# Optimization experiments

Hardware: AMD Instinct MI355X
Metric: run time of the kernel (lower is better)

## Reference

```python
import jax, jax.numpy as jnp
import numpy as np
import math

B, C, IMG, P = 16, 3, 512, 16
H = 384            # hidden_size
NH = 6             # num heads
DH = H // NH       # head dim = 64
L = 12             # layers
I = 1536           # intermediate
NC = 1000          # classes
NP = (IMG // P) ** 2          # 1024 patches
S = NP + 1                    # seq len with cls token
EPS = 1e-5
GELU_C = math.sqrt(2.0 / math.pi)


def setup_inputs() -> dict:
    key = jax.random.key(0)
    ks = iter(jax.random.split(key, 32))
    def rn(shape, scale=0.02):
        return (jax.random.normal(next(ks), shape, dtype=jnp.float32) * scale)
    return {
        "x": jax.random.normal(next(ks), (B, C, IMG, IMG), dtype=jnp.float32),
        "conv_w": rn((H, C, P, P)),
        "conv_b": rn((H,)),
        "cls_token": rn((1, 1, H), 1.0),
        "pos_emb": rn((1, S, H), 1.0),
        "ln1_w": jnp.ones((L, H), jnp.float32),
        "ln1_b": jnp.zeros((L, H), jnp.float32),
        "wq": rn((L, H, H)), "bq": rn((L, H)),
        "wk": rn((L, H, H)), "bk": rn((L, H)),
        "wv": rn((L, H, H)), "bv": rn((L, H)),
        "wo": rn((L, H, H)), "bo": rn((L, H)),
        "ln2_w": jnp.ones((L, H), jnp.float32),
        "ln2_b": jnp.zeros((L, H), jnp.float32),
        "w1": rn((L, H, I)), "b1": rn((L, I)),
        "w2": rn((L, I, H)), "b2": rn((L, H)),
        "wc": rn((H, NC)), "bc": rn((NC,)),
    }


def _layernorm(h, w, b):
    mu = jnp.mean(h, axis=-1, keepdims=True)
    var = jnp.mean(jnp.square(h - mu), axis=-1, keepdims=True)
    return (h - mu) * jax.lax.rsqrt(var + EPS) * w + b


def _new_gelu(u):
    return 0.5 * u * (1.0 + jnp.tanh(GELU_C * (u + 0.044715 * u ** 3)))


def _block(h, p):
    (l1w, l1b, wq, bq, wk, bk, wv, bv, wo, bo, l2w, l2b, w1, b1, w2, b2) = p
    hn = _layernorm(h, l1w, l1b)
    q = (hn @ wq + bq).reshape(B, S, NH, DH)
    k = (hn @ wk + bk).reshape(B, S, NH, DH)
    v = (hn @ wv + bv).reshape(B, S, NH, DH)
    scores = jnp.einsum('bihd,bjhd->bhij', q, k) / math.sqrt(DH)
    probs = jax.nn.softmax(scores, axis=-1)
    attn = jnp.einsum('bhij,bjhd->bihd', probs, v).reshape(B, S, H)
    h = h + attn @ wo + bo
    hn = _layernorm(h, l2w, l2b)
    h = h + _new_gelu(hn @ w1 + b1) @ w2 + b2
    return h, None


def reference(x, conv_w, conv_b, cls_token, pos_emb,
              ln1_w, ln1_b, wq, bq, wk, bk, wv, bv, wo, bo,
              ln2_w, ln2_b, w1, b1, w2, b2, wc, bc):
    # Patch embed: stride==kernel conv as einsum over non-overlapping patches
    nh = IMG // P
    patches = x.reshape(B, C, nh, P, nh, P)
    emb = jnp.einsum('bcipjq,ocpq->bijo', patches, conv_w) + conv_b  # [B,nh,nh,H]
    emb = emb.reshape(B, NP, H)
    cls = jnp.broadcast_to(cls_token, (B, 1, H))
    h = jnp.concatenate([cls, emb], axis=1) + pos_emb  # [B,S,H]

    params = (ln1_w, ln1_b, wq, bq, wk, bk, wv, bv, wo, bo,
              ln2_w, ln2_b, w1, b1, w2, b2)
    h, _ = jax.lax.scan(_block, h, params)
    logits = h[:, 0] @ wc + bc  # [B, NC]
    return logits
```

## Files before the change

### kernel.cpp

```cpp
#include <hip/hip_runtime.h>
#include <hip/hip_bf16.h>
#include <math.h>

#define BB 16
#define HH 384
#define NHEAD 6
#define DH 64
#define LL 12
#define II 1536
#define NC 1000
#define SS 1025
#define MROWS (BB * SS)
#define MPAD  16512
#define KPATCH 768
#define MPATCH (BB * 1024)
#define QS 1152
#define SSP 1088

typedef __hip_bfloat16 bf16;
typedef __attribute__((ext_vector_type(8))) short bh8;
typedef __attribute__((ext_vector_type(4))) float f4x;

__device__ __forceinline__ void gload16(const bf16* g, bf16* l) {
    __builtin_amdgcn_global_load_lds(
        (const __attribute__((address_space(1))) unsigned int*)g,
        (__attribute__((address_space(3))) unsigned int*)l, 16, 0, 0);
}

__device__ __forceinline__ unsigned short bf16_bits(float f) {
    __hip_bfloat16 h = __float2bfloat16(f);
    return *reinterpret_cast<unsigned short*>(&h);
}
__device__ __forceinline__ ushort4 pack4_bf16(float a, float b, float c, float d) {
    ushort4 u;
    u.x = bf16_bits(a); u.y = bf16_bits(b); u.z = bf16_bits(c); u.w = bf16_bits(d);
    return u;
}

__global__ __launch_bounds__(256) void transpose_cast_kernel(
    const float* __restrict__ in, bf16* __restrict__ out, int K, int N, int ostride)
{
    __shared__ float tile[32][33];
    int l = blockIdx.z;
    const float* ip = in + (size_t)l * K * N;
    bf16* op = out + (size_t)l * ostride;
    int n0 = blockIdx.x * 32, k0 = blockIdx.y * 32;
    int tx = threadIdx.x & 31, ty = threadIdx.x >> 5;
    #pragma unroll
    for (int i = 0; i < 32; i += 8)
        tile[ty + i][tx] = ip[(size_t)(k0 + ty + i) * N + n0 + tx];
    __syncthreads();
    #pragma unroll
    for (int i = 0; i < 32; i += 8)
        op[(size_t)(n0 + ty + i) * K + k0 + tx] = __float2bfloat16(tile[tx][ty + i]);
}

__global__ __launch_bounds__(256) void cast_kernel(
    const float* __restrict__ in, bf16* __restrict__ out, int n)
{
    int i = blockIdx.x * 1024 + threadIdx.x * 4;
    if (i + 3 < n) {
        float4 v = *(const float4*)&in[i];
        out[i]   = __float2bfloat16(v.x);
        out[i+1] = __float2bfloat16(v.y);
        out[i+2] = __float2bfloat16(v.z);
        out[i+3] = __float2bfloat16(v.w);
    } else {
        for (int j = i; j < n; ++j) out[j] = __float2bfloat16(in[j]);
    }
}

__global__ __launch_bounds__(384) void bias_concat_kernel(
    const float* __restrict__ bq, const float* __restrict__ bk,
    const float* __restrict__ bv, float* __restrict__ cb)
{
    int l = blockIdx.x, t = threadIdx.x;
    cb[l * QS + t]       = bq[l * HH + t];
    cb[l * QS + 384 + t] = bk[l * HH + t];
    cb[l * QS + 768 + t] = bv[l * HH + t];
}

__global__ __launch_bounds__(256) void im2row_kernel(
    const float* __restrict__ x, bf16* __restrict__ Pm)
{
    size_t idx = ((size_t)blockIdx.x * 256 + threadIdx.x) * 8;
    int kk = (int)(idx % KPATCH);
    int m  = (int)(idx / KPATCH);
    int b = m >> 10, p = m & 1023;
    int c = kk >> 8, rem = kk & 255, py = rem >> 4, px = rem & 15;
    int pi = p >> 5, pj = p & 31;
    const float* src = &x[(((size_t)b * 3 + c) * 512 + pi * 16 + py) * 512 + pj * 16 + px];
    float4 a0 = *(const float4*)src;
    float4 a1 = *(const float4*)(src + 4);
    bf16 tmp[8];
    tmp[0] = __float2bfloat16(a0.x); tmp[1] = __float2bfloat16(a0.y);
    tmp[2] = __float2bfloat16(a0.z); tmp[3] = __float2bfloat16(a0.w);
    tmp[4] = __float2bfloat16(a1.x); tmp[5] = __float2bfloat16(a1.y);
    tmp[6] = __float2bfloat16(a1.z); tmp[7] = __float2bfloat16(a1.w);
    *(bh8*)&Pm[idx] = *(bh8*)tmp;
}

__global__ __launch_bounds__(384) void fill_cls_kernel(
    const float* __restrict__ cls, const float* __restrict__ pos, float* __restrict__ h)
{
    h[(size_t)blockIdx.x * SS * HH + threadIdx.x] = cls[threadIdx.x] + pos[threadIdx.x];
}

__global__ __launch_bounds__(256) void ln_kernel(
    const float* __restrict__ x, const float* __restrict__ w,
    const float* __restrict__ b, bf16* __restrict__ out, int nrows)
{
    int wave = threadIdx.x >> 6;
    int lane = threadIdx.x & 63;
    int row = blockIdx.x * 4 + wave;
    if (row >= nrows) return;
    const float* xr = x + (size_t)row * HH;
    float vals[6];
    float s = 0.f;
    #pragma unroll
    for (int i = 0; i < 6; ++i) { vals[i] = xr[lane + 64 * i]; s += vals[i]; }
    #pragma unroll
    for (int mask = 32; mask >= 1; mask >>= 1) s += __shfl_xor(s, mask);
    float mean = s * (1.f / HH);
    float vs = 0.f;
    #pragma unroll
    for (int i = 0; i < 6; ++i) { float d = vals[i] - mean; vs += d * d; }
    #pragma unroll
    for (int mask = 32; mask >= 1; mask >>= 1) vs += __shfl_xor(vs, mask);
    float rstd = rsqrtf(vs * (1.f / HH) + 1e-5f);
    bf16* outr = out + (size_t)row * HH;
    #pragma unroll
    for (int i = 0; i < 6; ++i) {
        int jj = lane + 64 * i;
        outr[jj] = __float2bfloat16((vals[i] - mean) * rstd * w[jj] + b[jj]);
    }
}

__global__ __launch_bounds__(256) void vt_kernel(
    const bf16* __restrict__ qkv, bf16* __restrict__ vt)
{
    __shared__ bf16 tile[32][33];
    int bh = blockIdx.z;
    int b = bh / NHEAD, hd = bh % NHEAD;
    int s0 = blockIdx.x * 32, d0 = blockIdx.y * 32;
    int tx = threadIdx.x & 31, ty = threadIdx.x >> 5;
    const bf16* src = qkv + ((size_t)b * SS) * QS + 768 + hd * DH;
    #pragma unroll
    for (int i = 0; i < 32; i += 8) {
        int s = s0 + ty + i;
        tile[ty + i][tx] = (s < SS) ? src[(size_t)s * QS + d0 + tx]
                                    : __float2bfloat16(0.f);
    }
    __syncthreads();
    #pragma unroll
    for (int i = 0; i < 32; i += 8)
        vt[((size_t)bh * DH + d0 + ty + i) * SSP + s0 + tx] = tile[tx][ty + i];
}

template<int MODE>
__global__ __launch_bounds__(256) void gemm_v2_kernel(
    const bf16* __restrict__ A, const bf16* __restrict__ Bt,
    const float* __restrict__ bias, const float* __restrict__ res,
    void* __restrict__ out, int M, int N, int K)
{
    __shared__ bf16 As[128 * 64];
    __shared__ bf16 Bs[128 * 64];

    int t = threadIdx.x;
    int w = t >> 6, lane = t & 63;
    int quad = lane >> 4, l15 = lane & 15;
    int bm = blockIdx.x * 128, bn = blockIdx.y * 128;
    int wm = (w >> 1) * 64, wn = (w & 1) * 64;

    int srow = lane >> 3;
    int scol = lane & 7;

    f4x acc[4][4];
    #pragma unroll
    for (int i = 0; i < 4; ++i)
        #pragma unroll
        for (int j = 0; j < 4; ++j) acc[i][j] = 0.f;

    for (int k0 = 0; k0 < K; k0 += 64) {
        #pragma unroll
        for (int p = 0; p < 4; ++p) {
            int c = w * 4 + p;
            int r = c * 8 + srow;
            int gcb = scol ^ (r & 7);
            gload16(A + (size_t)(bm + r) * K + k0 + gcb * 8, &As[c * 8 * 64]);
        }
        #pragma unroll
        for (int p = 0; p < 4; ++p) {
            int c = w * 4 + p;
            int r = c * 8 + srow;
            int gcb = scol ^ (r & 7);
            gload16(Bt + (size_t)(bn + r) * K + k0 + gcb * 8, &Bs[c * 8 * 64]);
        }
        __syncthreads();

        #pragma unroll
        for (int kc = 0; kc < 2; ++kc) {
            bh8 bfr[4];
            #pragma unroll
            for (int nf = 0; nf < 4; ++nf) {
                int rn = wn + nf * 16 + l15;
                int pcb = (kc * 4 + quad) ^ (rn & 7);
                bfr[nf] = *(const bh8*)&Bs[rn * 64 + pcb * 8];
            }
            #pragma unroll
            for (int mf = 0; mf < 4; ++mf) {
                int rm = wm + mf * 16 + l15;
                int pcb = (kc * 4 + quad) ^ (rm & 7);
                bh8 afr = *(const bh8*)&As[rm * 64 + pcb * 8];
                #pragma unroll
                for (int nf = 0; nf < 4; ++nf)
                    acc[mf][nf] = __builtin_amdgcn_mfma_f32_16x16x32_bf16(
                        bfr[nf], afr, acc[mf][nf], 0, 0, 0);
            }
        }
        __syncthreads();
    }

    #pragma unroll
    for (int mf = 0; mf < 4; ++mf) {
        int row = bm + wm + mf * 16 + l15;
        #pragma unroll
        for (int nf = 0; nf < 4; ++nf) {
            f4x v = acc[mf][nf];
            int col0 = bn + wn + nf * 16 + quad * 4;
            float4 b4 = *(const float4*)&bias[col0];
            float vals[4];
            #pragma unroll
            for (int r = 0; r < 4; ++r) vals[r] = v[r] + (&b4.x)[r];
            if (MODE == 0) {
                if (row < M)
                    *(ushort4*)&((bf16*)out)[(size_t)row * N + col0] =
                        pack4_bf16(vals[0], vals[1], vals[2], vals[3]);
            } else if (MODE == 1) {
                #pragma unroll
                for (int r = 0; r < 4; ++r) {
                    float u = vals[r];
                    float z = 0.7978845608028654f * (u + 0.044715f * u * u * u);
                    z = fminf(fmaxf(z, -15.f), 15.f);
                    float e = __expf(2.f * z);
                    vals[r] = 0.5f * u * (1.f + (e - 1.f) / (e + 1.f));
                }
                if (row < M)
                    *(ushort4*)&((bf16*)out)[(size_t)row * N + col0] =
                        pack4_bf16(vals[0], vals[1], vals[2], vals[3]);
            } else if (MODE == 2) {
                if (row < M) {
                    float* o = (float*)out;
                    float4 r4 = *(const float4*)&res[(size_t)row * N + col0];
                    float4 st = {vals[0] + r4.x, vals[1] + r4.y,
                                 vals[2] + r4.z, vals[3] + r4.w};
                    *(float4*)&o[(size_t)row * N + col0] = st;
                }
            } else {
                int b2 = row >> 10, p2 = row & 1023;
                size_t orow = (size_t)b2 * SS + 1 + p2;
                float4 r4 = *(const float4*)&res[(size_t)(1 + p2) * HH + col0];
                float4 st = {vals[0] + r4.x, vals[1] + r4.y,
                             vals[2] + r4.z, vals[3] + r4.w};
                *(float4*)&((float*)out)[orow * HH + col0] = st;
            }
        }
    }
}

#define PSTR 68

__global__ __launch_bounds__(256) void attn_v4_kernel(
    const bf16* __restrict__ qkv, const bf16* __restrict__ vt,
    bf16* __restrict__ o)
{
    __shared__ bf16 Qs[64 * 64];
    __shared__ bf16 Ks[64 * 64];
    __shared__ bf16 Vs[64 * 64];
    __shared__ bf16 Ps[4][16 * PSTR];

    int t = threadIdx.x, w = t >> 6, lane = t & 63;
    int quad = lane >> 4, l15 = lane & 15;
    int bh = blockIdx.x;
    int b = bh / NHEAD, hd = bh % NHEAD;
    int q0 = blockIdx.y * 64;
    size_t qbase = ((size_t)b * SS) * QS + hd * DH;
    size_t kbase = qbase + 384;
    size_t vbase = (size_t)bh * DH * SSP;
    size_t obase = ((size_t)b * SS) * HH + hd * DH;

    int srow = lane >> 3, scol = lane & 7;
    int gcb = scol ^ srow;

    #pragma unroll
    for (int p = 0; p < 2; ++p) {
        int c = w * 2 + p;
        int r = c * 8 + srow;
        gload16(qkv + qbase + (size_t)(q0 + r) * QS + gcb * 8, &Qs[c * 512]);
    }
    __syncthreads();

    bh8 qfrag[2];
    {
        int rm = 16 * w + l15;
        #pragma unroll
        for (int kc = 0; kc < 2; ++kc)
            qfrag[kc] = *(const bh8*)&Qs[rm * 64 + ((kc * 4 + quad) ^ (rm & 7)) * 8];
    }

    f4x oacc[4];
    #pragma unroll
    for (int i = 0; i < 4; ++i) oacc[i] = 0.f;
    float l_part = 0.f;

    const float C1 = 0.18033688011112042f;
    const float C2 = -16.0f;

    for (int c0 = 0; c0 < SS; c0 += 64) {
        __syncthreads();
        #pragma unroll
        for (int p = 0; p < 2; ++p) {
            int c = w * 2 + p;
            int r = c * 8 + srow;
            gload16(qkv + kbase + (size_t)(c0 + r) * QS + gcb * 8, &Ks[c * 512]);
            gload16(vt + vbase + (size_t)r * SSP + c0 + gcb * 8, &Vs[c * 512]);
        }
        __syncthreads();

        bool tail = (c0 + 64 > SS);
        #pragma unroll
        for (int nf = 0; nf < 4; ++nf) {
            f4x s = 0.f;
            int rn = nf * 16 + l15;
            #pragma unroll
            for (int kc = 0; kc < 2; ++kc) {
                bh8 kf = *(const bh8*)&Ks[rn * 64 + ((kc * 4 + quad) ^ (rn & 7)) * 8];
                s = __builtin_amdgcn_mfma_f32_16x16x32_bf16(kf, qfrag[kc], s, 0, 0, 0);
            }
            float pv[4];
            #pragma unroll
            for (int r = 0; r < 4; ++r) {
                float p = exp2f(fmaf(s[r], C1, C2));
                if (tail && (c0 + nf * 16 + quad * 4 + r >= SS)) p = 0.f;
                pv[r] = p;
                l_part += p;
            }
            *(ushort4*)&Ps[w][l15 * PSTR + nf * 16 + quad * 4] =
                pack4_bf16(pv[0], pv[1], pv[2], pv[3]);
        }

        bh8 pf[2];
        #pragma unroll
        for (int kc = 0; kc < 2; ++kc)
            pf[kc] = *(const bh8*)&Ps[w][l15 * PSTR + kc * 32 + quad * 8];

        #pragma unroll
        for (int nf2 = 0; nf2 < 4; ++nf2) {
            int rn2 = nf2 * 16 + l15;
            #pragma unroll
            for (int kc = 0; kc < 2; ++kc) {
                bh8 vf = *(const bh8*)&Vs[rn2 * 64 + ((kc * 4 + quad) ^ (rn2 & 7)) * 8];
                oacc[nf2] = __builtin_amdgcn_mfma_f32_16x16x32_bf16(vf, pf[kc], oacc[nf2], 0, 0, 0);
            }
        }
    }

    l_part += __shfl_xor(l_part, 16);
    l_part += __shfl_xor(l_part, 32);
    float inv = 1.f / l_part;

    int row = q0 + 16 * w + l15;
    if (row < SS) {
        #pragma unroll
        for (int nf2 = 0; nf2 < 4; ++nf2) {
            *(ushort4*)&o[obase + (size_t)row * HH + nf2 * 16 + quad * 4] =
                pack4_bf16(oacc[nf2][0] * inv, oacc[nf2][1] * inv,
                           oacc[nf2][2] * inv, oacc[nf2][3] * inv);
        }
    }
}

__global__ __launch_bounds__(256) void cls_kernel(
    const float* __restrict__ h, const float* __restrict__ wc,
    const float* __restrict__ bc, float* __restrict__ out)
{
    __shared__ float hr[HH];
    __shared__ float part[4][64];
    int b = blockIdx.y, n0 = blockIdx.x * 64;
    int t = threadIdx.x;
    for (int i = t; i < HH; i += 256) hr[i] = h[(size_t)b * SS * HH + i];
    __syncthreads();
    int nn = t & 63, seg = t >> 6;
    int n = n0 + nn;
    float acc = 0.f;
    if (n < NC) {
        #pragma unroll 4
        for (int kk = seg * 96; kk < seg * 96 + 96; ++kk)
            acc += hr[kk] * wc[(size_t)kk * NC + n];
    }
    part[seg][nn] = acc;
    __syncthreads();
    if (t < 64 && n0 + t < NC)
        out[b * NC + n0 + t] = part[0][t] + part[1][t] + part[2][t] + part[3][t] + bc[n0 + t];
}

extern "C" void kernel_launch(void* const* d_in, const int* in_sizes, int n_in,
                              void* d_out, int out_size, void* d_ws, size_t ws_size,
                              hipStream_t stream) {
    const float* x        = (const float*)d_in[0];
    const float* conv_w   = (const float*)d_in[1];
    const float* conv_b   = (const float*)d_in[2];
    const float* cls_tok  = (const float*)d_in[3];
    const float* pos_emb  = (const float*)d_in[4];
    const float* ln1_w    = (const float*)d_in[5];
    const float* ln1_b    = (const float*)d_in[6];
    const float* wq       = (const float*)d_in[7];
    const float* bq       = (const float*)d_in[8];
    const float* wk       = (const float*)d_in[9];
    const float* bk       = (const float*)d_in[10];
    const float* wv       = (const float*)d_in[11];
    const float* bv       = (const float*)d_in[12];
    const float* wo       = (const float*)d_in[13];
    const float* bo       = (const float*)d_in[14];
    const float* ln2_w    = (const float*)d_in[15];
    const float* ln2_b    = (const float*)d_in[16];
    const float* w1       = (const float*)d_in[17];
    const float* b1       = (const float*)d_in[18];
    const float* w2       = (const float*)d_in[19];
    const float* b2       = (const float*)d_in[20];
    const float* wc       = (const float*)d_in[21];
    const float* bc       = (const float*)d_in[22];
    float* out = (float*)d_out;

    char* wp = (char*)d_ws;
    float* h   = (float*)wp;  wp += (size_t)MROWS * HH * 4;
    bf16* hn   = (bf16*)wp;
    bf16* vtb  = (bf16*)wp;   wp += (size_t)96 * DH * SSP * 2;
    bf16* tb   = (bf16*)wp;   wp += (size_t)MPAD * HH * 2;
    bf16* mb   = (bf16*)wp;   wp += (size_t)MPAD * II * 2;
    bf16* qkvb = mb;
    bf16* Pm   = mb;
    bf16* wqkv = (bf16*)wp;   wp += (size_t)LL * QS * HH * 2;
    bf16* wot  = (bf16*)wp;   wp += (size_t)LL * HH * HH * 2;
    bf16* w1t  = (bf16*)wp;   wp += (size_t)LL * HH * II * 2;
    bf16* w2t  = (bf16*)wp;   wp += (size_t)LL * II * HH * 2;
    bf16* cwb  = (bf16*)wp;   wp += (size_t)HH * KPATCH * 2;
    float* cbias = (float*)wp; wp += (size_t)LL * QS * 4;

    transpose_cast_kernel<<<dim3(12, 12, LL), 256, 0, stream>>>(wq, wqkv,          HH, HH, QS * HH);
    transpose_cast_kernel<<<dim3(12, 12, LL), 256, 0, stream>>>(wk, wqkv + 147456, HH, HH, QS * HH);
    transpose_cast_kernel<<<dim3(12, 12, LL), 256, 0, stream>>>(wv, wqkv + 294912, HH, HH, QS * HH);
    transpose_cast_kernel<<<dim3(12, 12, LL), 256, 0, stream>>>(wo, wot, HH, HH, HH * HH);
    transpose_cast_kernel<<<dim3(48, 12, LL), 256, 0, stream>>>(w1, w1t, HH, II, HH * II);
    transpose_cast_kernel<<<dim3(12, 48, LL), 256, 0, stream>>>(w2, w2t, II, HH, II * HH);
    cast_kernel<<<288, 256, 0, stream>>>(conv_w, cwb, HH * KPATCH);
    bias_concat_kernel<<<LL, 384, 0, stream>>>(bq, bk, bv, cbias);

    im2row_kernel<<<6144, 256, 0, stream>>>(x, Pm);
    gemm_v2_kernel<3><<<dim3(128, 3), 256, 0, stream>>>(
        Pm, cwb, conv_b, pos_emb, h, MPATCH, HH, KPATCH);
    fill_cls_kernel<<<BB, 384, 0, stream>>>(cls_tok, pos_emb, h);

    const int M = MROWS;
    dim3 gQKV(129, 9);
    dim3 gH(129, 3);
    dim3 gI(129, 12);

    for (int l = 0; l < LL; ++l) {
        const float* l1w = ln1_w + (size_t)l * HH;
        const float* l1b = ln1_b + (size_t)l * HH;
        const float* l2w = ln2_w + (size_t)l * HH;
        const float* l2b = ln2_b + (size_t)l * HH;
        const bf16* wqkv_l = wqkv + (size_t)l * QS * HH;
        const bf16* wo_l   = wot  + (size_t)l * HH * HH;
        const bf16* w1_l   = w1t  + (size_t)l * HH * II;
        const bf16* w2_l   = w2t  + (size_t)l * II * HH;
        const float* cb_l  = cbias + (size_t)l * QS;
        const float* bo_l  = bo + (size_t)l * HH;
        const float* b1_l  = b1 + (size_t)l * II;
        const float* b2_l  = b2 + (size_t)l * HH;

        ln_kernel<<<4100, 256, 0, stream>>>(h, l1w, l1b, hn, M);

        gemm_v2_kernel<0><<<gQKV, 256, 0, stream>>>(hn, wqkv_l, cb_l, nullptr, qkvb, M, QS, HH);

        vt_kernel<<<dim3(33, 2, 96), 256, 0, stream>>>(qkvb, vtb);

        attn_v4_kernel<<<dim3(96, 17), 256, 0, stream>>>(qkvb, vtb, tb);

        gemm_v2_kernel<2><<<gH, 256, 0, stream>>>(tb, wo_l, bo_l, h, h, M, HH, HH);

        ln_kernel<<<4100, 256, 0, stream>>>(h, l2w, l2b, hn, M);

        gemm_v2_kernel<1><<<gI, 256, 0, stream>>>(hn, w1_l, b1_l, nullptr, mb, M, II, HH);
        gemm_v2_kernel<2><<<gH, 256, 0, stream>>>(mb, w2_l, b2_l, h, h, M, HH, II);
    }

    cls_kernel<<<dim3(16, BB), 256, 0, stream>>>(h, wc, bc, out);
}
```

Before: 3.264 ms.

## Process 128 query rows per attention block and compute softmax sum via MFMA

The attention kernel now handles two 64-row query bands per block, so each K/V tile loaded into LDS is reused twice and the grid drops from 17 to 9 query blocks. The row sum of probabilities is computed by an extra MFMA against a ones row appended to the V tile, replacing per-lane accumulation and shuffles. The Q and P buffers share one LDS region, and the tail mask is hoisted out of the common path. The trade-offs are fewer blocks per head, which lowers parallelism, and higher register pressure from doubled accumulators. The sum is also now taken from bf16-rounded probabilities.

Result: slower. 3.398 ms (+4.1%).

```diff
diff --git a/kernel.cpp b/kernel.cpp
--- a/kernel.cpp
+++ b/kernel.cpp
@@ -270,20 +270,19 @@
 
 #define PSTR 68
 
-__global__ __launch_bounds__(256) void attn_v4_kernel(
+__global__ __launch_bounds__(256) void attn_v5_kernel(
     const bf16* __restrict__ qkv, const bf16* __restrict__ vt,
     bf16* __restrict__ o)
 {
-    __shared__ bf16 Qs[64 * 64];
+    __shared__ bf16 QPs[8704];
     __shared__ bf16 Ks[64 * 64];
-    __shared__ bf16 Vs[64 * 64];
-    __shared__ bf16 Ps[4][16 * PSTR];
+    __shared__ bf16 Vs[80 * 64];
 
     int t = threadIdx.x, w = t >> 6, lane = t & 63;
     int quad = lane >> 4, l15 = lane & 15;
     int bh = blockIdx.x;
     int b = bh / NHEAD, hd = bh % NHEAD;
-    int q0 = blockIdx.y * 64;
+    int q0 = blockIdx.y * 128;
     size_t qbase = ((size_t)b * SS) * QS + hd * DH;
     size_t kbase = qbase + 384;
     size_t vbase = (size_t)bh * DH * SSP;
@@ -293,25 +292,32 @@
     int gcb = scol ^ srow;
 
     #pragma unroll
-    for (int p = 0; p < 2; ++p) {
-        int c = w * 2 + p;
+    for (int p = 0; p < 4; ++p) {
+        int c = w * 4 + p;
         int r = c * 8 + srow;
-        gload16(qkv + qbase + (size_t)(q0 + r) * QS + gcb * 8, &Qs[c * 512]);
-    }
+        gload16(qkv + qbase + (size_t)(q0 + r) * QS + gcb * 8, &QPs[c * 512]);
+    }
+    for (int i = t; i < 16 * 64; i += 256)
+        Vs[64 * 64 + i] = __float2bfloat16(i < 64 ? 1.f : 0.f);
     __syncthreads();
 
-    bh8 qfrag[2];
-    {
-        int rm = 16 * w + l15;
+    bh8 qfrag[2][2];
+    #pragma unroll
+    for (int band = 0; band < 2; ++band) {
+        int rm = band * 64 + 16 * w + l15;
         #pragma unroll
         for (int kc = 0; kc < 2; ++kc)
-            qfrag[kc] = *(const bh8*)&Qs[rm * 64 + ((kc * 4 + quad) ^ (rm & 7)) * 8];
-    }
-
-    f4x oacc[4];
-    #pragma unroll
-    for (int i = 0; i < 4; ++i) oacc[i] = 0.f;
-    float l_part = 0.f;
+            qfrag[band][kc] = *(const bh8*)&QPs[rm * 64 + ((kc * 4 + quad) ^ (rm & 7)) * 8];
+    }
+
+    f4x oacc[2][4];
+    f4x oacc_l[2];
+    #pragma unroll
+    for (int band = 0; band < 2; ++band) {
+        oacc_l[band] = 0.f;
+        #pragma unroll
+        for (int i = 0; i < 4; ++i) oacc[band][i] = 0.f;
+    }
 
     const float C1 = 0.18033688011112042f;
     const float C2 = -16.0f;
@@ -329,53 +335,66 @@
 
         bool tail = (c0 + 64 > SS);
         #pragma unroll
-        for (int nf = 0; nf < 4; ++nf) {
-            f4x s = 0.f;
-            int rn = nf * 16 + l15;
+        for (int band = 0; band < 2; ++band) {
+            bf16* Psb = &QPs[((w * 2 + band) * 16) * PSTR];
+
+            #pragma unroll
+            for (int nf = 0; nf < 4; ++nf) {
+                f4x s = 0.f;
+                int rn = nf * 16 + l15;
+                #pragma unroll
+                for (int kc = 0; kc < 2; ++kc) {
+                    bh8 kf = *(const bh8*)&Ks[rn * 64 + ((kc * 4 + quad) ^ (rn & 7)) * 8];
+                    s = __builtin_amdgcn_mfma_f32_16x16x32_bf16(kf, qfrag[band][kc], s, 0, 0, 0);
+                }
+                float pv[4];
+                if (tail) {
+                    #pragma unroll
+                    for (int r = 0; r < 4; ++r) {
+                        float p = exp2f(fmaf(s[r], C1, C2));
+                        pv[r] = (c0 + nf * 16 + quad * 4 + r < SS) ? p : 0.f;
+                    }
+                } else {
+                    #pragma unroll
+                    for (int r = 0; r < 4; ++r)
+                        pv[r] = exp2f(fmaf(s[r], C1, C2));
+                }
+                *(ushort4*)&Psb[l15 * PSTR + nf * 16 + quad * 4] =
+                    pack4_bf16(pv[0], pv[1], pv[2], pv[3]);
+            }
+
+            bh8 pf[2];
+            #pragma unroll
+            for (int kc = 0; kc < 2; ++kc)
+                pf[kc] = *(const bh8*)&Psb[l15 * PSTR + kc * 32 + quad * 8];
+
             #pragma unroll
             for (int kc = 0; kc < 2; ++kc) {
-                bh8 kf = *(const bh8*)&Ks[rn * 64 + ((kc * 4 + quad) ^ (rn & 7)) * 8];
-                s = __builtin_amdgcn_mfma_f32_16x16x32_bf16(kf, qfrag[kc], s, 0, 0, 0);
+                #pragma unroll
+                for (int nf2 = 0; nf2 < 4; ++nf2) {
+                    int rn2 = nf2 * 16 + l15;
+                    bh8 vf = *(const bh8*)&Vs[rn2 * 64 + ((kc * 4 + quad) ^ (rn2 & 7)) * 8];
+                    oacc[band][nf2] = __builtin_amdgcn_mfma_f32_16x16x32_bf16(
+                        vf, pf[kc], oacc[band][nf2], 0, 0, 0);
+                }
+                bh8 vf1 = *(const bh8*)&Vs[(64 + l15) * 64 + ((kc * 4 + quad) ^ (l15 & 7)) * 8];
+                oacc_l[band] = __builtin_amdgcn_mfma_f32_16x16x32_bf16(
+                    vf1, pf[kc], oacc_l[band], 0, 0, 0);
             }
-            float pv[4];
-            #pragma unroll
-            for (int r = 0; r < 4; ++r) {
-                float p = exp2f(fmaf(s[r], C1, C2));
-                if (tail && (c0 + nf * 16 + quad * 4 + r >= SS)) p = 0.f;
-                pv[r] = p;
-                l_part += p;
-            }
-            *(ushort4*)&Ps[w][l15 * PSTR + nf * 16 + quad * 4] =
-                pack4_bf16(pv[0], pv[1], pv[2], pv[3]);
-        }
-
-        bh8 pf[2];
-        #pragma unroll
-        for (int kc = 0; kc < 2; ++kc)
-            pf[kc] = *(const bh8*)&Ps[w][l15 * PSTR + kc * 32 + quad * 8];
-
-        #pragma unroll
-        for (int nf2 = 0; nf2 < 4; ++nf2) {
-            int rn2 = nf2 * 16 + l15;
-            #pragma unroll
-            for (int kc = 0; kc < 2; ++kc) {
-                bh8 vf = *(const bh8*)&Vs[rn2 * 64 + ((kc * 4 + quad) ^ (rn2 & 7)) * 8];
-                oacc[nf2] = __builtin_amdgcn_mfma_f32_16x16x32_bf16(vf, pf[kc], oacc[nf2], 0, 0, 0);
-            }
-        }
-    }
-
-    l_part += __shfl_xor(l_part, 16);
-    l_part += __shfl_xor(l_part, 32);
-    float inv = 1.f / l_part;
-
-    int row = q0 + 16 * w + l15;
-    if (row < SS) {
-        #pragma unroll
-        for (int nf2 = 0; nf2 < 4; ++nf2) {
-            *(ushort4*)&o[obase + (size_t)row * HH + nf2 * 16 + quad * 4] =
-                pack4_bf16(oacc[nf2][0] * inv, oacc[nf2][1] * inv,
-                           oacc[nf2][2] * inv, oacc[nf2][3] * inv);
+        }
+    }
+
+    #pragma unroll
+    for (int band = 0; band < 2; ++band) {
+        float l_val = __shfl(oacc_l[band][0], l15);
+        float inv = 1.f / l_val;
+        int row = q0 + band * 64 + 16 * w + l15;
+        if (row < SS) {
+            #pragma unroll
+            for (int nf2 = 0; nf2 < 4; ++nf2)
+                *(ushort4*)&o[obase + (size_t)row * HH + nf2 * 16 + quad * 4] =
+                    pack4_bf16(oacc[band][nf2][0] * inv, oacc[band][nf2][1] * inv,
+                               oacc[band][nf2][2] * inv, oacc[band][nf2][3] * inv);
         }
     }
 }
@@ -486,7 +505,7 @@
 
         vt_kernel<<<dim3(33, 2, 96), 256, 0, stream>>>(qkvb, vtb);
 
-        attn_v4_kernel<<<dim3(96, 17), 256, 0, stream>>>(qkvb, vtb, tb);
+        attn_v5_kernel<<<dim3(96, 9), 256, 0, stream>>>(qkvb, vtb, tb);
 
         gemm_v2_kernel<2><<<gH, 256, 0, stream>>>(tb, wo_l, bo_l, h, h, M, HH, HH);
 
```

## Fuse V transpose into QKV GEMM epilogue and double-buffer attention K/V tiles

Applied to the files above, without the earlier changes.

Removes the separate V-transpose kernel by having the QKV GEMM epilogue also write V in transposed layout, and gives the attention kernel double-buffered K/V shared-memory tiles so the next tile's loads overlap compute, with one barrier per iteration. It also splits the non-tail exp path from the masked path. This saves a launch and a read/write pass over V, but adds scattered 2-byte strided stores in the GEMM epilogue. The padded sequence tail of the transposed V buffer is no longer zero-filled, since hn no longer aliases it.

After: 3.146 ms. -3.6%, faster.

```diff
diff --git a/kernel.cpp b/kernel.cpp
--- a/kernel.cpp
+++ b/kernel.cpp
@@ -136,32 +136,11 @@
     }
 }
 
-__global__ __launch_bounds__(256) void vt_kernel(
-    const bf16* __restrict__ qkv, bf16* __restrict__ vt)
-{
-    __shared__ bf16 tile[32][33];
-    int bh = blockIdx.z;
-    int b = bh / NHEAD, hd = bh % NHEAD;
-    int s0 = blockIdx.x * 32, d0 = blockIdx.y * 32;
-    int tx = threadIdx.x & 31, ty = threadIdx.x >> 5;
-    const bf16* src = qkv + ((size_t)b * SS) * QS + 768 + hd * DH;
-    #pragma unroll
-    for (int i = 0; i < 32; i += 8) {
-        int s = s0 + ty + i;
-        tile[ty + i][tx] = (s < SS) ? src[(size_t)s * QS + d0 + tx]
-                                    : __float2bfloat16(0.f);
-    }
-    __syncthreads();
-    #pragma unroll
-    for (int i = 0; i < 32; i += 8)
-        vt[((size_t)bh * DH + d0 + ty + i) * SSP + s0 + tx] = tile[tx][ty + i];
-}
-
 template<int MODE>
 __global__ __launch_bounds__(256) void gemm_v2_kernel(
     const bf16* __restrict__ A, const bf16* __restrict__ Bt,
     const float* __restrict__ bias, const float* __restrict__ res,
-    void* __restrict__ out, int M, int N, int K)
+    void* __restrict__ out, bf16* __restrict__ vtout, int M, int N, int K)
 {
     __shared__ bf16 As[128 * 64];
     __shared__ bf16 Bs[128 * 64];
@@ -232,11 +211,7 @@
             float vals[4];
             #pragma unroll
             for (int r = 0; r < 4; ++r) vals[r] = v[r] + (&b4.x)[r];
-            if (MODE == 0) {
-                if (row < M)
-                    *(ushort4*)&((bf16*)out)[(size_t)row * N + col0] =
-                        pack4_bf16(vals[0], vals[1], vals[2], vals[3]);
-            } else if (MODE == 1) {
+            if (MODE == 1) {
                 #pragma unroll
                 for (int r = 0; r < 4; ++r) {
                     float u = vals[r];
@@ -256,13 +231,30 @@
                                  vals[2] + r4.z, vals[3] + r4.w};
                     *(float4*)&o[(size_t)row * N + col0] = st;
                 }
-            } else {
+            } else if (MODE == 3) {
                 int b2 = row >> 10, p2 = row & 1023;
                 size_t orow = (size_t)b2 * SS + 1 + p2;
                 float4 r4 = *(const float4*)&res[(size_t)(1 + p2) * HH + col0];
                 float4 st = {vals[0] + r4.x, vals[1] + r4.y,
                              vals[2] + r4.z, vals[3] + r4.w};
                 *(float4*)&((float*)out)[orow * HH + col0] = st;
+            } else {
+                if (row < M) {
+                    *(ushort4*)&((bf16*)out)[(size_t)row * N + col0] =
+                        pack4_bf16(vals[0], vals[1], vals[2], vals[3]);
+                    if (col0 >= 768) {
+                        int b2 = row / 1025;
+                        int s  = row - b2 * 1025;
+                        int dg = col0 - 768;
+                        int hd2 = dg >> 6, dd = dg & 63;
+                        bf16* vp = vtout +
+                            ((size_t)((b2 * NHEAD + hd2) * DH + dd)) * SSP + s;
+                        vp[0]       = __float2bfloat16(vals[0]);
+                        vp[SSP]     = __float2bfloat16(vals[1]);
+                        vp[2 * SSP] = __float2bfloat16(vals[2]);
+                        vp[3 * SSP] = __float2bfloat16(vals[3]);
+                    }
+                }
             }
         }
     }
@@ -270,13 +262,13 @@
 
 #define PSTR 68
 
-__global__ __launch_bounds__(256) void attn_v4_kernel(
+__global__ __launch_bounds__(256) void attn_v6_kernel(
     const bf16* __restrict__ qkv, const bf16* __restrict__ vt,
     bf16* __restrict__ o)
 {
     __shared__ bf16 Qs[64 * 64];
-    __shared__ bf16 Ks[64 * 64];
-    __shared__ bf16 Vs[64 * 64];
+    __shared__ bf16 Ks[2][64 * 64];
+    __shared__ bf16 Vs[2][64 * 64];
     __shared__ bf16 Ps[4][16 * PSTR];
 
     int t = threadIdx.x, w = t >> 6, lane = t & 63;
@@ -297,6 +289,8 @@
         int c = w * 2 + p;
         int r = c * 8 + srow;
         gload16(qkv + qbase + (size_t)(q0 + r) * QS + gcb * 8, &Qs[c * 512]);
+        gload16(qkv + kbase + (size_t)r * QS + gcb * 8, &Ks[0][c * 512]);
+        gload16(vt + vbase + (size_t)r * SSP + gcb * 8, &Vs[0][c * 512]);
     }
     __syncthreads();
 
@@ -316,16 +310,22 @@
     const float C1 = 0.18033688011112042f;
     const float C2 = -16.0f;
 
-    for (int c0 = 0; c0 < SS; c0 += 64) {
-        __syncthreads();
-        #pragma unroll
-        for (int p = 0; p < 2; ++p) {
-            int c = w * 2 + p;
-            int r = c * 8 + srow;
-            gload16(qkv + kbase + (size_t)(c0 + r) * QS + gcb * 8, &Ks[c * 512]);
-            gload16(vt + vbase + (size_t)r * SSP + c0 + gcb * 8, &Vs[c * 512]);
-        }
-        __syncthreads();
+    const int NT = (SS + 63) / 64;
+    for (int it = 0; it < NT; ++it) {
+        int cur = it & 1;
+        int c0 = it * 64;
+
+        if (it + 1 < NT) {
+            int nxt = cur ^ 1;
+            int c1 = c0 + 64;
+            #pragma unroll
+            for (int p = 0; p < 2; ++p) {
+                int c = w * 2 + p;
+                int r = c * 8 + srow;
+                gload16(qkv + kbase + (size_t)(c1 + r) * QS + gcb * 8, &Ks[nxt][c * 512]);
+                gload16(vt + vbase + (size_t)r * SSP + c1 + gcb * 8, &Vs[nxt][c * 512]);
+            }
+        }
 
         bool tail = (c0 + 64 > SS);
         #pragma unroll
@@ -334,17 +334,23 @@
             int rn = nf * 16 + l15;
             #pragma unroll
             for (int kc = 0; kc < 2; ++kc) {
-                bh8 kf = *(const bh8*)&Ks[rn * 64 + ((kc * 4 + quad) ^ (rn & 7)) * 8];
+                bh8 kf = *(const bh8*)&Ks[cur][rn * 64 + ((kc * 4 + quad) ^ (rn & 7)) * 8];
                 s = __builtin_amdgcn_mfma_f32_16x16x32_bf16(kf, qfrag[kc], s, 0, 0, 0);
             }
             float pv[4];
-            #pragma unroll
-            for (int r = 0; r < 4; ++r) {
-                float p = exp2f(fmaf(s[r], C1, C2));
-                if (tail && (c0 + nf * 16 + quad * 4 + r >= SS)) p = 0.f;
-                pv[r] = p;
-                l_part += p;
-            }
+            if (tail) {
+                #pragma unroll
+                for (int r = 0; r < 4; ++r) {
+                    float p = exp2f(fmaf(s[r], C1, C2));
+                    pv[r] = (c0 + nf * 16 + quad * 4 + r < SS) ? p : 0.f;
+                }
+            } else {
+                #pragma unroll
+                for (int r = 0; r < 4; ++r)
+                    pv[r] = exp2f(fmaf(s[r], C1, C2));
+            }
+            #pragma unroll
+            for (int r = 0; r < 4; ++r) l_part += pv[r];
             *(ushort4*)&Ps[w][l15 * PSTR + nf * 16 + quad * 4] =
                 pack4_bf16(pv[0], pv[1], pv[2], pv[3]);
         }
@@ -359,10 +365,12 @@
             int rn2 = nf2 * 16 + l15;
             #pragma unroll
             for (int kc = 0; kc < 2; ++kc) {
-                bh8 vf = *(const bh8*)&Vs[rn2 * 64 + ((kc * 4 + quad) ^ (rn2 & 7)) * 8];
+                bh8 vf = *(const bh8*)&Vs[cur][rn2 * 64 + ((kc * 4 + quad) ^ (rn2 & 7)) * 8];
                 oacc[nf2] = __builtin_amdgcn_mfma_f32_16x16x32_bf16(vf, pf[kc], oacc[nf2], 0, 0, 0);
             }
         }
+
+        __syncthreads();
     }
 
     l_part += __shfl_xor(l_part, 16);
@@ -372,11 +380,10 @@
     int row = q0 + 16 * w + l15;
     if (row < SS) {
         #pragma unroll
-        for (int nf2 = 0; nf2 < 4; ++nf2) {
+        for (int nf2 = 0; nf2 < 4; ++nf2)
             *(ushort4*)&o[obase + (size_t)row * HH + nf2 * 16 + quad * 4] =
                 pack4_bf16(oacc[nf2][0] * inv, oacc[nf2][1] * inv,
                            oacc[nf2][2] * inv, oacc[nf2][3] * inv);
-        }
     }
 }
 
@@ -434,7 +441,7 @@
 
     char* wp = (char*)d_ws;
     float* h   = (float*)wp;  wp += (size_t)MROWS * HH * 4;
-    bf16* hn   = (bf16*)wp;
+    bf16* hn   = (bf16*)wp;   wp += (size_t)MPAD * HH * 2;
     bf16* vtb  = (bf16*)wp;   wp += (size_t)96 * DH * SSP * 2;
     bf16* tb   = (bf16*)wp;   wp += (size_t)MPAD * HH * 2;
     bf16* mb   = (bf16*)wp;   wp += (size_t)MPAD * II * 2;
@@ -458,7 +465,7 @@
 
     im2row_kernel<<<6144, 256, 0, stream>>>(x, Pm);
     gemm_v2_kernel<3><<<dim3(128, 3), 256, 0, stream>>>(
-        Pm, cwb, conv_b, pos_emb, h, MPATCH, HH, KPATCH);
+        Pm, cwb, conv_b, pos_emb, h, nullptr, MPATCH, HH, KPATCH);
     fill_cls_kernel<<<BB, 384, 0, stream>>>(cls_tok, pos_emb, h);
 
     const int M = MROWS;
@@ -482,18 +489,16 @@
 
         ln_kernel<<<4100, 256, 0, stream>>>(h, l1w, l1b, hn, M);
 
-        gemm_v2_kernel<0><<<gQKV, 256, 0, stream>>>(hn, wqkv_l, cb_l, nullptr, qkvb, M, QS, HH);
-
-        vt_kernel<<<dim3(33, 2, 96), 256, 0, stream>>>(qkvb, vtb);
-
-        attn_v4_kernel<<<dim3(96, 17), 256, 0, stream>>>(qkvb, vtb, tb);
-
-        gemm_v2_kernel<2><<<gH, 256, 0, stream>>>(tb, wo_l, bo_l, h, h, M, HH, HH);
+        gemm_v2_kernel<4><<<gQKV, 256, 0, stream>>>(hn, wqkv_l, cb_l, nullptr, qkvb, vtb, M, QS, HH);
+
+        attn_v6_kernel<<<dim3(96, 17), 256, 0, stream>>>(qkvb, vtb, tb);
+
+        gemm_v2_kernel<2><<<gH, 256, 0, stream>>>(tb, wo_l, bo_l, h, h, nullptr, M, HH, HH);
 
         ln_kernel<<<4100, 256, 0, stream>>>(h, l2w, l2b, hn, M);
 
-        gemm_v2_kernel<1><<<gI, 256, 0, stream>>>(hn, w1_l, b1_l, nullptr, mb, M, II, HH);
-        gemm_v2_kernel<2><<<gH, 256, 0, stream>>>(mb, w2_l, b2_l, h, h, M, HH, II);
+        gemm_v2_kernel<1><<<gI, 256, 0, stream>>>(hn, w1_l, b1_l, nullptr, mb, nullptr, M, II, HH);
+        gemm_v2_kernel<2><<<gH, 256, 0, stream>>>(mb, w2_l, b2_l, h, h, nullptr, M, HH, II);
     }
 
     cls_kernel<<<dim3(16, BB), 256, 0, stream>>>(h, wc, bc, out);
```
